# Kernel optimization log

Measured on AMD Instinct MI355X. Metric: run time of the kernel, lower is better.

The kernel has to match this reference:

```python
import jax, jax.numpy as jnp
import numpy as np

EMBED_DIM = 1024
NUM_HEADS = 16
HEAD_DIM = EMBED_DIM // NUM_HEADS


def setup_inputs() -> dict:
    key = jax.random.key(0)
    k1, k2, k3, k4, k5 = jax.random.split(key, 5)
    B, S, D = 4, 2048, EMBED_DIM
    scale = 1.0 / np.sqrt(D)
    qkv = jax.random.normal(k1, (B, S, D), dtype=jnp.float32)
    W_in = jax.random.uniform(k2, (D, 3 * D), dtype=jnp.float32, minval=-scale, maxval=scale)
    b_in = jax.random.uniform(k3, (3 * D,), dtype=jnp.float32, minval=-scale, maxval=scale)
    W_out = jax.random.uniform(k4, (D, D), dtype=jnp.float32, minval=-scale, maxval=scale)
    b_out = jax.random.uniform(k5, (D,), dtype=jnp.float32, minval=-scale, maxval=scale)
    return {"qkv": qkv, "W_in": W_in, "b_in": b_in, "W_out": W_out, "b_out": b_out}


def reference(qkv, W_in, b_in, W_out, b_out):
    B, S, D = qkv.shape
    H, hd = NUM_HEADS, HEAD_DIM
    proj = qkv @ W_in + b_in                      # [B, S, 3D]
    q, k, v = jnp.split(proj, 3, axis=-1)         # each [B, S, D]
    # reshape to heads: [B, H, S, hd]
    q = q.reshape(B, S, H, hd).transpose(0, 2, 1, 3)
    k = k.reshape(B, S, H, hd).transpose(0, 2, 1, 3)
    v = v.reshape(B, S, H, hd).transpose(0, 2, 1, 3)
    scores = jnp.einsum('bhqd,bhkd->bhqk', q, k) / jnp.sqrt(jnp.float32(hd))
    attn = jax.nn.softmax(scores, axis=-1)        # dropout=0.0 -> identity
    ctx = jnp.einsum('bhqk,bhkd->bhqd', attn, v)  # [B, H, S, hd]
    ctx = ctx.transpose(0, 2, 1, 3).reshape(B, S, D)
    return ctx @ W_out + b_out
```

## Files before the change

### kernel.cpp

```cpp
#include <hip/hip_runtime.h>


typedef __bf16 bf16;
typedef __bf16 bf16x4 __attribute__((ext_vector_type(4)));
typedef __bf16 bf16x8 __attribute__((ext_vector_type(8)));
typedef float f32x4 __attribute__((ext_vector_type(4)));

typedef const __attribute__((address_space(1))) void* gas1p;
typedef __attribute__((address_space(3))) void* las3p;
#define GLD16(g, l) __builtin_amdgcn_global_load_lds((gas1p)(g), (las3p)(l), 16, 0, 0)

#if __has_builtin(__builtin_amdgcn_exp2f)
#define EXP2(x) __builtin_amdgcn_exp2f(x)
#else
#define EXP2(x) exp2f(x)
#endif

__device__ __forceinline__ f32x4 mfma16(bf16x8 a, bf16x8 b, f32x4 c) {
  return __builtin_amdgcn_mfma_f32_16x16x32_bf16(a, b, c, 0, 0, 0);
}

__global__ void cast_kernel(const float* __restrict__ in, bf16* __restrict__ out, int n) {
  int i = (blockIdx.x * 256 + threadIdx.x) * 4;
  if (i < n) {
    float4 v = *(const float4*)(in + i);
    bf16x4 o;
    o[0] = (bf16)v.x; o[1] = (bf16)v.y; o[2] = (bf16)v.z; o[3] = (bf16)v.w;
    *(bf16x4*)(out + i) = o;
  }
}

__global__ void transpose_cast_kernel(const float* __restrict__ in, bf16* __restrict__ out,
                                      int R, int C) {
  __shared__ float tile[32][33];
  int c0 = blockIdx.x * 32, r0 = blockIdx.y * 32;
  int tx = threadIdx.x, ty = threadIdx.y;
#pragma unroll
  for (int i = 0; i < 4; ++i)
    tile[ty + i * 8][tx] = in[(size_t)(r0 + ty + i * 8) * C + c0 + tx];
  __syncthreads();
#pragma unroll
  for (int i = 0; i < 4; ++i)
    out[(size_t)(c0 + ty + i * 8) * R + r0 + tx] = (bf16)tile[tx][ty + i * 8];
}

__global__ __launch_bounds__(256, 2) void gemm1_kernel(
    const bf16* __restrict__ A, const bf16* __restrict__ Bt, const float* __restrict__ bias,
    bf16* __restrict__ Qo, bf16* __restrict__ Ko, bf16* __restrict__ Vo) {
  __shared__ __align__(16) char sA[128 * 64 * 2];
  __shared__ __align__(16) char sB[128 * 64 * 2];
  const int tid = threadIdx.x, lane = tid & 63, wave = tid >> 6, quad = lane >> 4;
  const int m0 = blockIdx.y * 128, n0 = blockIdx.x * 128;
  const int wm = (wave >> 1) * 64, wn = (wave & 1) * 64;
  f32x4 acc[4][4] = {};

  for (int kt = 0; kt < 1024; kt += 64) {
    __syncthreads();
#pragma unroll
    for (int i = 0; i < 4; ++i) {
      int chunk = i * 256 + tid;
      int row = chunk >> 3;
      int cs = (chunk & 7) ^ (row & 7);
      GLD16(A + (size_t)(m0 + row) * 1024 + kt + cs * 8, sA + chunk * 16);
      GLD16(Bt + (size_t)(n0 + row) * 1024 + kt + cs * 8, sB + chunk * 16);
    }
    __syncthreads();
#pragma unroll
    for (int ks = 0; ks < 2; ++ks) {
      bf16x8 af[4], bfr[4];
#pragma unroll
      for (int t = 0; t < 4; ++t) {
        int ra = wm + t * 16 + (lane & 15);
        af[t] = *(const bf16x8*)(sA + ra * 128 + ((ks * 4 + quad) ^ (ra & 7)) * 16);
        int rb = wn + t * 16 + (lane & 15);
        bfr[t] = *(const bf16x8*)(sB + rb * 128 + ((ks * 4 + quad) ^ (rb & 7)) * 16);
      }
#pragma unroll
      for (int mt = 0; mt < 4; ++mt)
#pragma unroll
        for (int nt = 0; nt < 4; ++nt)
          acc[mt][nt] = mfma16(af[mt], bfr[nt], acc[mt][nt]);
    }
  }

  const int region = n0 >> 10;
#pragma unroll
  for (int nt = 0; nt < 4; ++nt) {
    int n = n0 + wn + nt * 16 + (lane & 15);
    float bv = bias[n];
    int ncol = n & 1023;
    int h = ncol >> 6, d = ncol & 63;
#pragma unroll
    for (int mt = 0; mt < 4; ++mt) {
      int gm = m0 + wm + mt * 16 + quad * 4;
      int bb = gm >> 11, s = gm & 2047;
      if (region == 2) {
        bf16x4 pk;
#pragma unroll
        for (int r = 0; r < 4; ++r) pk[r] = (bf16)(acc[mt][nt][r] + bv);
        *(bf16x4*)(Vo + ((size_t)((bb * 16 + h) * 64 + d)) * 2048 + s) = pk;
      } else {
        bf16* dst = (region == 0) ? Qo : Ko;
        float scl = (region == 0) ? 0.18033688f : 1.0f;
#pragma unroll
        for (int r = 0; r < 4; ++r)
          dst[((size_t)((bb * 16 + h) * 2048) + s + r) * 64 + d] =
              (bf16)((acc[mt][nt][r] + bv) * scl);
      }
    }
  }
}

__global__ __launch_bounds__(256, 2) void flash_kernel(
    const bf16* __restrict__ Q, const bf16* __restrict__ K, const bf16* __restrict__ Vt,
    bf16* __restrict__ ctx) {
  const int n = blockIdx.x;
  const int bh = (n & 7) * 8 + (n >> 6);
  const int qt = (n >> 3) & 7;
  const int b = bh >> 4, h = bh & 15;
  const int tid = threadIdx.x, lane = tid & 63, wave = tid >> 6, quad = lane >> 4;

  __shared__ __align__(16) char sK[2][128 * 64 * 2];
  __shared__ __align__(16) char sV[2][64 * 128 * 2];
  __shared__ __align__(16) char sP[4][64 * 32 * 2];

  const size_t hb = (size_t)bh * 2048 * 64;
  const int q0 = qt * 256;

#pragma unroll
  for (int i = 0; i < 8; ++i) {
    int chunk = i * 256 + tid;
    int row = chunk >> 3;
    int cs = (chunk & 7) ^ (row & 7);
    char* dst = (i < 4) ? (sK[0] + chunk * 16) : (sK[1] + (chunk - 1024) * 16);
    GLD16(Q + hb + (size_t)(q0 + row) * 64 + cs * 8, dst);
  }
  __syncthreads();
  bf16x8 qf[4][2];
#pragma unroll
  for (int j = 0; j < 4; ++j)
#pragma unroll
    for (int ksd = 0; ksd < 2; ++ksd) {
      int row = wave * 64 + j * 16 + (lane & 15);
      const char* src = sK[row >> 7];
      int r128 = row & 127;
      qf[j][ksd] = *(const bf16x8*)(src + r128 * 128 + ((ksd * 4 + quad) ^ (r128 & 7)) * 16);
    }
  __syncthreads();

#pragma unroll
  for (int i = 0; i < 4; ++i) {
    int chunk = i * 256 + tid;
    int row = chunk >> 3;
    int cs = (chunk & 7) ^ (row & 7);
    GLD16(K + hb + (size_t)row * 64 + cs * 8, sK[0] + chunk * 16);
    int vrow = chunk >> 4;
    int vcs = (chunk & 15) ^ (vrow & 7);
    GLD16(Vt + hb + (size_t)vrow * 2048 + vcs * 8, sV[0] + chunk * 16);
  }
  __syncthreads();

  f32x4 ctxa[4][4] = {};
  float l[4] = {0.f, 0.f, 0.f, 0.f};
  char* pw = sP[wave];

  for (int it = 0; it < 16; ++it) {
    const int kv0 = it * 128;
    if (it < 15) {
      char* nk = sK[(it + 1) & 1];
      char* nv = sV[(it + 1) & 1];
#pragma unroll
      for (int i = 0; i < 4; ++i) {
        int chunk = i * 256 + tid;
        int row = chunk >> 3;
        int cs = (chunk & 7) ^ (row & 7);
        GLD16(K + hb + (size_t)(kv0 + 128 + row) * 64 + cs * 8, nk + chunk * 16);
        int vrow = chunk >> 4;
        int vcs = (chunk & 15) ^ (vrow & 7);
        GLD16(Vt + hb + (size_t)vrow * 2048 + kv0 + 128 + vcs * 8, nv + chunk * 16);
      }
    }
    const char* cb = sK[it & 1];
    const char* vb = sV[it & 1];

#pragma unroll
    for (int kq = 0; kq < 4; ++kq) {
      f32x4 st[2][4] = {};
#pragma unroll
      for (int ksd = 0; ksd < 2; ++ksd) {
        bf16x8 kf[2];
#pragma unroll
        for (int ii = 0; ii < 2; ++ii) {
          int row = kq * 32 + ii * 16 + (lane & 15);
          kf[ii] = *(const bf16x8*)(cb + row * 128 + ((ksd * 4 + quad) ^ (row & 7)) * 16);
        }
#pragma unroll
        for (int ii = 0; ii < 2; ++ii)
#pragma unroll
          for (int j = 0; j < 4; ++j)
            st[ii][j] = mfma16(kf[ii], qf[j][ksd], st[ii][j]);
      }
#pragma unroll
      for (int ii = 0; ii < 2; ++ii)
#pragma unroll
        for (int j = 0; j < 4; ++j) {
          f32x4 p;
#pragma unroll
          for (int r = 0; r < 4; ++r) {
            p[r] = EXP2(st[ii][j][r]);
            l[j] += p[r];
          }
          bf16x4 pk;
#pragma unroll
          for (int r = 0; r < 4; ++r) pk[r] = (bf16)p[r];
          int q = j * 16 + (lane & 15);
          int chunk = ii * 2 + (quad >> 1);
          *(bf16x4*)(pw + q * 64 + ((chunk ^ (q & 3)) * 16) + (quad & 1) * 8) = pk;
        }
      bf16x8 pf[4], vf[4];
#pragma unroll
      for (int mt = 0; mt < 4; ++mt) {
        int q = mt * 16 + (lane & 15);
        pf[mt] = *(const bf16x8*)(pw + q * 64 + ((quad ^ (q & 3)) * 16));
      }
#pragma unroll
      for (int nd = 0; nd < 4; ++nd) {
        int row = nd * 16 + (lane & 15);
        vf[nd] = *(const bf16x8*)(vb + row * 256 + (((kq * 4 + quad) ^ (row & 7)) * 16));
      }
#pragma unroll
      for (int mt = 0; mt < 4; ++mt)
#pragma unroll
        for (int nd = 0; nd < 4; ++nd)
          ctxa[mt][nd] = mfma16(pf[mt], vf[nd], ctxa[mt][nd]);
    }
    __syncthreads();
  }

#pragma unroll
  for (int j = 0; j < 4; ++j) {
    l[j] += __shfl_xor(l[j], 16);
    l[j] += __shfl_xor(l[j], 32);
  }
#pragma unroll
  for (int mt = 0; mt < 4; ++mt)
#pragma unroll
    for (int r = 0; r < 4; ++r) {
      float lsh = __shfl(l[mt], quad * 4 + r);
      float rl = __builtin_amdgcn_rcpf(lsh);
      int srow = q0 + wave * 64 + mt * 16 + quad * 4 + r;
#pragma unroll
      for (int nd = 0; nd < 4; ++nd) {
        int col = h * 64 + nd * 16 + (lane & 15);
        ctx[((size_t)(b * 2048 + srow)) * 1024 + col] = (bf16)(ctxa[mt][nd][r] * rl);
      }
    }
}

__global__ __launch_bounds__(256, 2) void gemm2_kernel(
    const bf16* __restrict__ A, const bf16* __restrict__ Bt, const float* __restrict__ bias,
    float* __restrict__ Out) {
  __shared__ __align__(16) char sA[128 * 64 * 2];
  __shared__ __align__(16) char sB[128 * 64 * 2];
  const int tid = threadIdx.x, lane = tid & 63, wave = tid >> 6, quad = lane >> 4;
  const int m0 = blockIdx.y * 128, n0 = blockIdx.x * 128;
  const int wm = (wave >> 1) * 64, wn = (wave & 1) * 64;
  f32x4 acc[4][4] = {};

  for (int kt = 0; kt < 1024; kt += 64) {
    __syncthreads();
#pragma unroll
    for (int i = 0; i < 4; ++i) {
      int chunk = i * 256 + tid;
      int row = chunk >> 3;
      int cs = (chunk & 7) ^ (row & 7);
      GLD16(A + (size_t)(m0 + row) * 1024 + kt + cs * 8, sA + chunk * 16);
      GLD16(Bt + (size_t)(n0 + row) * 1024 + kt + cs * 8, sB + chunk * 16);
    }
    __syncthreads();
#pragma unroll
    for (int ks = 0; ks < 2; ++ks) {
      bf16x8 af[4], bfr[4];
#pragma unroll
      for (int t = 0; t < 4; ++t) {
        int ra = wm + t * 16 + (lane & 15);
        af[t] = *(const bf16x8*)(sA + ra * 128 + ((ks * 4 + quad) ^ (ra & 7)) * 16);
        int rb = wn + t * 16 + (lane & 15);
        bfr[t] = *(const bf16x8*)(sB + rb * 128 + ((ks * 4 + quad) ^ (rb & 7)) * 16);
      }
#pragma unroll
      for (int mt = 0; mt < 4; ++mt)
#pragma unroll
        for (int nt = 0; nt < 4; ++nt)
          acc[mt][nt] = mfma16(af[mt], bfr[nt], acc[mt][nt]);
    }
  }

#pragma unroll
  for (int nt = 0; nt < 4; ++nt) {
    int n = n0 + wn + nt * 16 + (lane & 15);
    float bv = bias[n];
#pragma unroll
    for (int mt = 0; mt < 4; ++mt) {
      int gm = m0 + wm + mt * 16 + quad * 4;
#pragma unroll
      for (int r = 0; r < 4; ++r)
        Out[(size_t)(gm + r) * 1024 + n] = acc[mt][nt][r] + bv;
    }
  }
}

extern "C" void kernel_launch(void* const* d_in, const int* in_sizes, int n_in,
                              void* d_out, int out_size, void* d_ws, size_t ws_size,
                              hipStream_t stream) {
  const float* qkv   = (const float*)d_in[0];
  const float* W_in  = (const float*)d_in[1];
  const float* b_in  = (const float*)d_in[2];
  const float* W_out = (const float*)d_in[3];
  const float* b_out = (const float*)d_in[4];
  float* out = (float*)d_out;

  bf16* Xb    = (bf16*)d_ws;
  bf16* WtIn  = Xb + 8388608;
  bf16* WtOut = WtIn + 3145728;
  bf16* Qb    = WtOut + 1048576;
  bf16* Kb    = Qb + 8388608;
  bf16* Vtb   = Kb + 8388608;
  bf16* Ctx   = Xb;

  cast_kernel<<<8192, 256, 0, stream>>>(qkv, Xb, 8388608);
  transpose_cast_kernel<<<dim3(96, 32), dim3(32, 8), 0, stream>>>(W_in, WtIn, 1024, 3072);
  transpose_cast_kernel<<<dim3(32, 32), dim3(32, 8), 0, stream>>>(W_out, WtOut, 1024, 1024);
  gemm1_kernel<<<dim3(24, 64), 256, 0, stream>>>(Xb, WtIn, b_in, Qb, Kb, Vtb);
  flash_kernel<<<512, 256, 0, stream>>>(Qb, Kb, Vtb, Ctx);
  gemm2_kernel<<<dim3(8, 64), 256, 0, stream>>>(Ctx, WtOut, b_out, out);
}
```

Baseline: 265.2 us.

## Double-buffer LDS tiles in both projection GEMMs to overlap loads with MFMA

Both projection GEMM kernels now use two LDS buffers per operand. The next K-tile is issued via global_load_lds into the spare buffer while MFMAs run on the current one, with a single barrier per step instead of two. This is meant to hide global-to-LDS latency behind compute. It doubles LDS use to 64 KB per block, which may reduce occupancy.

```diff
diff --git a/kernel.cpp b/kernel.cpp
--- a/kernel.cpp
+++ b/kernel.cpp
@@ -44,43 +44,63 @@
     out[(size_t)(c0 + ty + i * 8) * R + r0 + tx] = (bf16)tile[tx][ty + i * 8];
 }
 
+__device__ __forceinline__ void stage_tile(const bf16* __restrict__ src, size_t rstride,
+                                           int kt, char* dst, int tid) {
+#pragma unroll
+  for (int i = 0; i < 4; ++i) {
+    int chunk = i * 256 + tid;
+    int row = chunk >> 3;
+    int cs = (chunk & 7) ^ (row & 7);
+    GLD16(src + (size_t)row * rstride + kt + cs * 8, dst + chunk * 16);
+  }
+}
+
+__device__ __forceinline__ void gemm_step(
+    const bf16* __restrict__ A, const bf16* __restrict__ B, int m0, int n0,
+    const char* ca, const char* cb, char* na, char* nb, int ktn, bool pref,
+    int tid, int lane, int quad, int wm, int wn, f32x4 (&acc)[4][4]) {
+  if (pref) {
+    stage_tile(A + (size_t)m0 * 1024, 1024, ktn, na, tid);
+    stage_tile(B + (size_t)n0 * 1024, 1024, ktn, nb, tid);
+  }
+#pragma unroll
+  for (int ks = 0; ks < 2; ++ks) {
+    bf16x8 af[4], bfr[4];
+#pragma unroll
+    for (int t = 0; t < 4; ++t) {
+      int ra = wm + t * 16 + (lane & 15);
+      af[t] = *(const bf16x8*)(ca + ra * 128 + ((ks * 4 + quad) ^ (ra & 7)) * 16);
+      int rb = wn + t * 16 + (lane & 15);
+      bfr[t] = *(const bf16x8*)(cb + rb * 128 + ((ks * 4 + quad) ^ (rb & 7)) * 16);
+    }
+#pragma unroll
+    for (int mt = 0; mt < 4; ++mt)
+#pragma unroll
+      for (int nt = 0; nt < 4; ++nt)
+        acc[mt][nt] = mfma16(af[mt], bfr[nt], acc[mt][nt]);
+  }
+  __syncthreads();
+}
+
 __global__ __launch_bounds__(256, 2) void gemm1_kernel(
     const bf16* __restrict__ A, const bf16* __restrict__ Bt, const float* __restrict__ bias,
     bf16* __restrict__ Qo, bf16* __restrict__ Ko, bf16* __restrict__ Vo) {
-  __shared__ __align__(16) char sA[128 * 64 * 2];
-  __shared__ __align__(16) char sB[128 * 64 * 2];
-  const int tid = threadIdx.x, lane = tid & 63, wave = tid >> 6, quad = lane >> 4;
+  __shared__ __align__(16) char sA[2][128 * 64 * 2];
+  __shared__ __align__(16) char sB[2][128 * 64 * 2];
+  const int tid = threadIdx.x, lane = tid & 63, quad = lane >> 4;
+  const int wave = tid >> 6;
   const int m0 = blockIdx.y * 128, n0 = blockIdx.x * 128;
   const int wm = (wave >> 1) * 64, wn = (wave & 1) * 64;
   f32x4 acc[4][4] = {};
 
-  for (int kt = 0; kt < 1024; kt += 64) {
-    __syncthreads();
-#pragma unroll
-    for (int i = 0; i < 4; ++i) {
-      int chunk = i * 256 + tid;
-      int row = chunk >> 3;
-      int cs = (chunk & 7) ^ (row & 7);
-      GLD16(A + (size_t)(m0 + row) * 1024 + kt + cs * 8, sA + chunk * 16);
-      GLD16(Bt + (size_t)(n0 + row) * 1024 + kt + cs * 8, sB + chunk * 16);
-    }
-    __syncthreads();
-#pragma unroll
-    for (int ks = 0; ks < 2; ++ks) {
-      bf16x8 af[4], bfr[4];
-#pragma unroll
-      for (int t = 0; t < 4; ++t) {
-        int ra = wm + t * 16 + (lane & 15);
-        af[t] = *(const bf16x8*)(sA + ra * 128 + ((ks * 4 + quad) ^ (ra & 7)) * 16);
-        int rb = wn + t * 16 + (lane & 15);
-        bfr[t] = *(const bf16x8*)(sB + rb * 128 + ((ks * 4 + quad) ^ (rb & 7)) * 16);
-      }
-#pragma unroll
-      for (int mt = 0; mt < 4; ++mt)
-#pragma unroll
-        for (int nt = 0; nt < 4; ++nt)
-          acc[mt][nt] = mfma16(af[mt], bfr[nt], acc[mt][nt]);
-    }
+  stage_tile(A + (size_t)m0 * 1024, 1024, 0, sA[0], tid);
+  stage_tile(Bt + (size_t)n0 * 1024, 1024, 0, sB[0], tid);
+  __syncthreads();
+  for (int it = 0; it < 16; it += 2) {
+    gemm_step(A, Bt, m0, n0, sA[0], sB[0], sA[1], sB[1], (it + 1) * 64, true,
+              tid, lane, quad, wm, wn, acc);
+    gemm_step(A, Bt, m0, n0, sA[1], sB[1], sA[0], sB[0], (it + 2) * 64, it + 2 < 16,
+              tid, lane, quad, wm, wn, acc);
   }
 
   const int region = n0 >> 10;
@@ -260,40 +280,22 @@
 __global__ __launch_bounds__(256, 2) void gemm2_kernel(
     const bf16* __restrict__ A, const bf16* __restrict__ Bt, const float* __restrict__ bias,
     float* __restrict__ Out) {
-  __shared__ __align__(16) char sA[128 * 64 * 2];
-  __shared__ __align__(16) char sB[128 * 64 * 2];
-  const int tid = threadIdx.x, lane = tid & 63, wave = tid >> 6, quad = lane >> 4;
+  __shared__ __align__(16) char sA[2][128 * 64 * 2];
+  __shared__ __align__(16) char sB[2][128 * 64 * 2];
+  const int tid = threadIdx.x, lane = tid & 63, quad = lane >> 4;
+  const int wave = tid >> 6;
   const int m0 = blockIdx.y * 128, n0 = blockIdx.x * 128;
   const int wm = (wave >> 1) * 64, wn = (wave & 1) * 64;
   f32x4 acc[4][4] = {};
 
-  for (int kt = 0; kt < 1024; kt += 64) {
-    __syncthreads();
-#pragma unroll
-    for (int i = 0; i < 4; ++i) {
-      int chunk = i * 256 + tid;
-      int row = chunk >> 3;
-      int cs = (chunk & 7) ^ (row & 7);
-      GLD16(A + (size_t)(m0 + row) * 1024 + kt + cs * 8, sA + chunk * 16);
-      GLD16(Bt + (size_t)(n0 + row) * 1024 + kt + cs * 8, sB + chunk * 16);
-    }
-    __syncthreads();
-#pragma unroll
-    for (int ks = 0; ks < 2; ++ks) {
-      bf16x8 af[4], bfr[4];
-#pragma unroll
-      for (int t = 0; t < 4; ++t) {
-        int ra = wm + t * 16 + (lane & 15);
-        af[t] = *(const bf16x8*)(sA + ra * 128 + ((ks * 4 + quad) ^ (ra & 7)) * 16);
-        int rb = wn + t * 16 + (lane & 15);
-        bfr[t] = *(const bf16x8*)(sB + rb * 128 + ((ks * 4 + quad) ^ (rb & 7)) * 16);
-      }
-#pragma unroll
-      for (int mt = 0; mt < 4; ++mt)
-#pragma unroll
-        for (int nt = 0; nt < 4; ++nt)
-          acc[mt][nt] = mfma16(af[mt], bfr[nt], acc[mt][nt]);
-    }
+  stage_tile(A + (size_t)m0 * 1024, 1024, 0, sA[0], tid);
+  stage_tile(Bt + (size_t)n0 * 1024, 1024, 0, sB[0], tid);
+  __syncthreads();
+  for (int it = 0; it < 16; it += 2) {
+    gemm_step(A, Bt, m0, n0, sA[0], sB[0], sA[1], sB[1], (it + 1) * 64, true,
+              tid, lane, quad, wm, wn, acc);
+    gemm_step(A, Bt, m0, n0, sA[1], sB[1], sA[0], sB[0], (it + 2) * 64, it + 2 < 16,
+              tid, lane, quad, wm, wn, acc);
   }
 
 #pragma unroll
```

Measured after the change: 264.2 us. No clear change (-0.4%).
